# Kernel tuning notes

Measured on AMD Instinct MI355X. Metric: run time of the kernel, lower is better.

Reference implementation:

```python
import jax, jax.numpy as jnp
import numpy as np

H = 100  # hidden size
EPS = 1e-5  # BatchNorm1d default eps


def setup_inputs() -> dict:
    key = jax.random.key(0)
    ks = jax.random.split(key, 9)
    s_ih = 1.0 / np.sqrt(H)
    inp = {
        "x": jax.random.normal(ks[0], (16, 4096, 40), dtype=jnp.float32),
        "W_ih": jax.random.uniform(ks[1], (4 * H, 40), jnp.float32, -s_ih, s_ih),
        "W_hh": jax.random.uniform(ks[2], (4 * H, H), jnp.float32, -s_ih, s_ih),
        "b_ih": jax.random.uniform(ks[3], (4 * H,), jnp.float32, -s_ih, s_ih),
        "b_hh": jax.random.uniform(ks[4], (4 * H,), jnp.float32, -s_ih, s_ih),
        "W1": jax.random.uniform(ks[5], (H, H), jnp.float32, -s_ih, s_ih),
        "b1": jax.random.uniform(ks[6], (H,), jnp.float32, -s_ih, s_ih),
        "gamma": jnp.ones((H,), jnp.float32),
        "beta": jnp.zeros((H,), jnp.float32),
        "W2": jax.random.uniform(ks[7], (40, H), jnp.float32, -s_ih, s_ih),
        "b2": jax.random.uniform(ks[8], (40,), jnp.float32, -s_ih, s_ih),
    }
    return inp


def _lstm_last_h(x, W_ih, W_hh, b_ih, b_hh):
    # x: [B, T, 40] -> precompute input projections for all timesteps
    B = x.shape[0]
    xg = jnp.einsum("bti,gi->tbg", x, W_ih) + b_ih + b_hh  # [T, B, 4H]
    W_hh_T = W_hh.T  # [H, 4H]

    def step(carry, xg_t):
        h, c = carry
        z = xg_t + h @ W_hh_T  # [B, 4H]
        i = jax.nn.sigmoid(z[:, 0 * H:1 * H])
        f = jax.nn.sigmoid(z[:, 1 * H:2 * H])
        g = jnp.tanh(z[:, 2 * H:3 * H])
        o = jax.nn.sigmoid(z[:, 3 * H:4 * H])
        c = f * c + i * g
        h = o * jnp.tanh(c)
        return (h, c), None

    h0 = jnp.zeros((B, H), x.dtype)
    c0 = jnp.zeros((B, H), x.dtype)
    (h_T, _), _ = jax.lax.scan(step, (h0, c0), xg)
    return h_T  # [B, H] == out[:, -1, :]


def reference(x, W_ih, W_hh, b_ih, b_hh, W1, b1, gamma, beta, W2, b2):
    h = _lstm_last_h(x, W_ih, W_hh, b_ih, b_hh)  # [B, H]
    y = h @ W1.T + b1  # Linear(100, 100)
    # BatchNorm1d in training mode: batch statistics, biased variance
    mu = jnp.mean(y, axis=0)
    var = jnp.mean((y - mu) ** 2, axis=0)
    y = (y - mu) * jax.lax.rsqrt(var + EPS) * gamma + beta
    y = y @ W2.T + b2  # Linear(100, 40)
    return y.reshape(-1, 10, 4)
```

## Files before the change

kernel.cpp:

```cpp
#include <hip/hip_runtime.h>
#include <cstddef>
#include <cstdint>

#define H100  100
#define G4    400
#define BATCH 16
#define TTOT  4096
#define NIN   40

__device__ __forceinline__ float fast_rcp(float x) { return __builtin_amdgcn_rcpf(x); }

__device__ __forceinline__ float gate_act(float z, bool is_g) {
    float m = is_g ? -2.0f : -1.0f;
    float e = __expf(m * z);
    float r = fast_rcp(1.0f + e);
    return is_g ? (2.0f * r - 1.0f) : r;
}
__device__ __forceinline__ float tanh_fast(float x) {
    float e = __expf(-2.0f * x);
    float r = fast_rcp(1.0f + e);
    return 2.0f * r - 1.0f;
}

__global__ __launch_bounds__(256) void xg_kernel(
    const float* __restrict__ x, const float* __restrict__ W_ih,
    const float* __restrict__ b_ih, const float* __restrict__ b_hh,
    float* __restrict__ xg, int t0, int steps, int chunkT)
{
    __shared__ float W_lds[NIN * G4];
    __shared__ float x_lds[16 * NIN];
    __shared__ float bias_lds[G4];

    int tid = threadIdx.x;
    int blocks_per_b = (steps + 15) >> 4;
    int b   = blockIdx.x / blocks_per_b;
    int tt  = blockIdx.x % blocks_per_b;
    int lt0 = tt * 16;
    int ntau = min(16, steps - lt0);

    for (int p = tid; p < NIN * G4; p += 256) {
        int g = p / NIN, i = p % NIN;
        W_lds[i * G4 + g] = W_ih[p];
    }
    for (int p = tid; p < G4; p += 256) bias_lds[p] = b_ih[p] + b_hh[p];
    const float* xsrc = x + ((size_t)b * TTOT + (size_t)(t0 + lt0)) * NIN;
    for (int p = tid; p < ntau * NIN; p += 256) x_lds[p] = xsrc[p];
    __syncthreads();

    int ntask = ntau * G4;
    for (int p = tid; p < ntask; p += 256) {
        int tau = p / G4, g = p % G4;
        float acc = bias_lds[g];
        #pragma unroll
        for (int i = 0; i < NIN; i++)
            acc = fmaf(x_lds[tau * NIN + i], W_lds[i * G4 + g], acc);
        xg[((size_t)b * chunkT + (size_t)(lt0 + tau)) * G4 + g] = acc;
    }
}

using h2_t = decltype(__builtin_amdgcn_cvt_pkrtz(0.0f, 0.0f));

__device__ __forceinline__ int h2i(h2_t v) { int r; __builtin_memcpy(&r, &v, 4); return r; }
__device__ __forceinline__ h2_t i2h(int v) { h2_t r; __builtin_memcpy(&r, &v, 4); return r; }

#if __has_builtin(__builtin_amdgcn_fdot2)
__device__ __forceinline__ float fdot2(h2_t a, h2_t b, float c) {
    return __builtin_amdgcn_fdot2(a, b, c, false);
}
#else
__device__ __forceinline__ float fdot2(h2_t a, h2_t b, float c) {
    float d;
    asm("v_dot2_f32_f16 %0, %1, %2, %3" : "=v"(d) : "v"(a), "v"(b), "v"(c));
    return d;
}
#endif

#define PIN2(a, b) asm volatile("" : "+v"(a), "+v"(b))

__global__ __launch_bounds__(256)
__attribute__((amdgpu_waves_per_eu(1, 1)))
void lstm_kernel(
    const float* __restrict__ xg, const float* __restrict__ W_hh,
    float* __restrict__ hc, int t0, int steps, int chunkT)
{
    __shared__ float a_lds[2][G4];

    const int x = threadIdx.x;
    const int b = blockIdx.x;
    const int l = x & 63;
    const bool hasB = (x < G4 - 256);
    const int  rA = x;
    const int  rB = hasB ? (x + 256) : 0;

    const float2* wra2 = (const float2*)(W_hh + (size_t)rA * H100);
    const float2* wrb2 = (const float2*)(W_hh + (size_t)rB * H100);
#define LDW(q) \
    int wa##q = h2i(__builtin_amdgcn_cvt_pkrtz(wra2[q].x, wra2[q].y)); \
    int wb##q = h2i(__builtin_amdgcn_cvt_pkrtz(wrb2[q].x, wrb2[q].y)); \
    PIN2(wa##q, wb##q);
    LDW(0)  LDW(1)  LDW(2)  LDW(3)  LDW(4)  LDW(5)  LDW(6)  LDW(7)
    LDW(8)  LDW(9)  LDW(10) LDW(11) LDW(12) LDW(13) LDW(14) LDW(15)
    LDW(16) LDW(17) LDW(18) LDW(19) LDW(20) LDW(21) LDW(22) LDW(23)
    LDW(24) LDW(25) LDW(26) LDW(27) LDW(28) LDW(29) LDW(30) LDW(31)
    LDW(32) LDW(33) LDW(34) LDW(35) LDW(36) LDW(37) LDW(38) LDW(39)
    LDW(40) LDW(41) LDW(42) LDW(43) LDW(44) LDW(45) LDW(46) LDW(47)
    LDW(48) LDW(49)
#undef LDW

    float* hch = hc;
    float* hcc = hc + BATCH * H100;

    float h0 = 0.f, h1 = 0.f, c0 = 0.f, c1 = 0.f;
    int hpi = 0;
    if (l < 50) {
        if (t0 != 0) {
            float2 hv = ((const float2*)(hch + b * H100))[l];
            float2 cv = ((const float2*)(hcc + b * H100))[l];
            h0 = hv.x; h1 = hv.y; c0 = cv.x; c1 = cv.y;
        }
        hpi = h2i(__builtin_amdgcn_cvt_pkrtz(h0, h1));
    }

    const float* xgb = xg + (size_t)b * chunkT * G4;
    float xcA = xgb[rA];
    float xcB = hasB ? xgb[rB] : 0.0f;

    const bool is_gA = (x >= 200) && (x < 300);
    const bool is_gB = (x < 44);

#define RLH2(src, idx) i2h(__builtin_amdgcn_readlane((src), (idx)))
#define DOTQ(q, aA, aB) { const h2_t u = RLH2(hpi, q); \
    aA = fdot2(i2h(wa##q), u, aA); \
    aB = fdot2(i2h(wb##q), u, aB); }

    #pragma unroll 1
    for (int t = 0; t < steps; t++) {
        float nxA = 0.f, nxB = 0.f;
        if (t + 1 < steps) {
            const float* p = xgb + (size_t)(t + 1) * G4;
            nxA = p[rA];
            nxB = p[rB];
        }

        float aA0 = 0, aA1 = 0, aB0 = 0, aB1 = 0;
        DOTQ(0,  aA0, aB0) DOTQ(1,  aA1, aB1) DOTQ(2,  aA0, aB0) DOTQ(3,  aA1, aB1)
        DOTQ(4,  aA0, aB0) DOTQ(5,  aA1, aB1) DOTQ(6,  aA0, aB0) DOTQ(7,  aA1, aB1)
        DOTQ(8,  aA0, aB0) DOTQ(9,  aA1, aB1) DOTQ(10, aA0, aB0) DOTQ(11, aA1, aB1)
        DOTQ(12, aA0, aB0) DOTQ(13, aA1, aB1) DOTQ(14, aA0, aB0) DOTQ(15, aA1, aB1)
        DOTQ(16, aA0, aB0) DOTQ(17, aA1, aB1) DOTQ(18, aA0, aB0) DOTQ(19, aA1, aB1)
        DOTQ(20, aA0, aB0) DOTQ(21, aA1, aB1) DOTQ(22, aA0, aB0) DOTQ(23, aA1, aB1)
        DOTQ(24, aA0, aB0) DOTQ(25, aA1, aB1) DOTQ(26, aA0, aB0) DOTQ(27, aA1, aB1)
        DOTQ(28, aA0, aB0) DOTQ(29, aA1, aB1) DOTQ(30, aA0, aB0) DOTQ(31, aA1, aB1)
        DOTQ(32, aA0, aB0) DOTQ(33, aA1, aB1) DOTQ(34, aA0, aB0) DOTQ(35, aA1, aB1)
        DOTQ(36, aA0, aB0) DOTQ(37, aA1, aB1) DOTQ(38, aA0, aB0) DOTQ(39, aA1, aB1)
        DOTQ(40, aA0, aB0) DOTQ(41, aA1, aB1) DOTQ(42, aA0, aB0) DOTQ(43, aA1, aB1)
        DOTQ(44, aA0, aB0) DOTQ(45, aA1, aB1) DOTQ(46, aA0, aB0) DOTQ(47, aA1, aB1)
        DOTQ(48, aA0, aB0) DOTQ(49, aA1, aB1)

        float zA = xcA + (aA0 + aA1);
        float zB = xcB + (aB0 + aB1);

        const int par = t & 1;
        a_lds[par][rA] = gate_act(zA, is_gA);
        if (hasB) a_lds[par][x + 256] = gate_act(zB, is_gB);
        __syncthreads();

        if (l < 50) {
            const float* ab = a_lds[par];
            float2 gi = ((const float2*)(ab))[l];
            float2 gf = ((const float2*)(ab + 100))[l];
            float2 gg = ((const float2*)(ab + 200))[l];
            float2 go = ((const float2*)(ab + 300))[l];
            c0 = fmaf(gf.x, c0, gi.x * gg.x);
            c1 = fmaf(gf.y, c1, gi.y * gg.y);
            h0 = go.x * tanh_fast(c0);
            h1 = go.y * tanh_fast(c1);
            hpi = h2i(__builtin_amdgcn_cvt_pkrtz(h0, h1));
        }
        xcA = nxA; xcB = nxB;
    }

    if (x < 64 && l < 50) {
        float2 hv = make_float2(h0, h1);
        float2 cv = make_float2(c0, c1);
        ((float2*)(hch + b * H100))[l] = hv;
        ((float2*)(hcc + b * H100))[l] = cv;
    }
#undef DOTQ
#undef RLH2
}

__global__ __launch_bounds__(256) void head_kernel(
    const float* __restrict__ hc, const float* __restrict__ W1,
    const float* __restrict__ b1, const float* __restrict__ gamma,
    const float* __restrict__ beta, const float* __restrict__ W2,
    const float* __restrict__ b2, float* __restrict__ out)
{
    __shared__ float h_s[BATCH * H100];
    __shared__ float W1_s[H100 * 101];
    __shared__ float y1_s[BATCH * H100];
    __shared__ float W2_s[40 * 101];
    __shared__ float scale_s[H100], shift_s[H100];

    int tid = threadIdx.x;
    for (int p = tid; p < BATCH * H100; p += 256) h_s[p] = hc[p];
    for (int p = tid; p < H100 * H100; p += 256)
        W1_s[(p / H100) * 101 + p % H100] = W1[p];
    for (int p = tid; p < 40 * H100; p += 256)
        W2_s[(p / H100) * 101 + p % H100] = W2[p];
    __syncthreads();

    for (int p = tid; p < BATCH * H100; p += 256) {
        int b = p / H100, j = p % H100;
        float acc = b1[j];
        for (int k = 0; k < H100; k++)
            acc = fmaf(h_s[b * H100 + k], W1_s[j * 101 + k], acc);
        y1_s[b * H100 + j] = acc;
    }
    __syncthreads();

    if (tid < H100) {
        float mu = 0.0f;
        for (int b = 0; b < BATCH; b++) mu += y1_s[b * H100 + tid];
        mu *= (1.0f / BATCH);
        float var = 0.0f;
        for (int b = 0; b < BATCH; b++) {
            float d = y1_s[b * H100 + tid] - mu;
            var = fmaf(d, d, var);
        }
        var *= (1.0f / BATCH);
        float sc = gamma[tid] * rsqrtf(var + 1e-5f);
        scale_s[tid] = sc;
        shift_s[tid] = beta[tid] - mu * sc;
    }
    __syncthreads();

    for (int p = tid; p < BATCH * 40; p += 256) {
        int b = p / 40, o = p % 40;
        float acc = b2[o];
        for (int k = 0; k < H100; k++)
            acc = fmaf(fmaf(y1_s[b * H100 + k], scale_s[k], shift_s[k]),
                       W2_s[o * 101 + k], acc);
        out[p] = acc;
    }
}

extern "C" void kernel_launch(void* const* d_in, const int* in_sizes, int n_in,
                              void* d_out, int out_size, void* d_ws, size_t ws_size,
                              hipStream_t stream)
{
    const float* x     = (const float*)d_in[0];
    const float* W_ih  = (const float*)d_in[1];
    const float* W_hh  = (const float*)d_in[2];
    const float* b_ih  = (const float*)d_in[3];
    const float* b_hh  = (const float*)d_in[4];
    const float* W1    = (const float*)d_in[5];
    const float* b1    = (const float*)d_in[6];
    const float* gamma = (const float*)d_in[7];
    const float* beta  = (const float*)d_in[8];
    const float* W2    = (const float*)d_in[9];
    const float* b2    = (const float*)d_in[10];
    float* out = (float*)d_out;

    float* hc = (float*)d_ws;
    float* xg = (float*)((char*)d_ws + 16384);
    size_t avail    = ws_size > 16384 ? ws_size - 16384 : 0;
    size_t per_step = (size_t)BATCH * G4 * sizeof(float);
    size_t ct       = (avail / per_step) & ~(size_t)15;
    int chunkT = ct > TTOT ? TTOT : (int)ct;
    if (chunkT < 16) chunkT = 16;

    for (int t0 = 0; t0 < TTOT; t0 += chunkT) {
        int steps = (TTOT - t0 < chunkT) ? (TTOT - t0) : chunkT;
        int bpb = (steps + 15) / 16;
        xg_kernel<<<dim3(BATCH * bpb), 256, 0, stream>>>(
            x, W_ih, b_ih, b_hh, xg, t0, steps, chunkT);
        lstm_kernel<<<dim3(BATCH), 256, 0, stream>>>(
            xg, W_hh, hc, t0, steps, chunkT);
    }
    head_kernel<<<1, 256, 0, stream>>>(hc, W1, b1, gamma, beta, W2, b2, out);
}
```

Before: 2.725 ms.

## Spread LSTM gate rows over 512 threads, one row per thread

The recurrent kernel now launches 512 threads per batch element, and each thread owns a single gate row instead of some threads owning two. This halves the dot-product chain per thread in the serial per-timestep critical path. The readlane broadcasts are software-pipelined ahead of their fdot2 uses. The cost is eight waves per block with a full barrier each step, and a 448-thread worker cutoff that leaves the last wave idle but still synchronising.

```diff
diff --git a/kernel.cpp b/kernel.cpp
--- a/kernel.cpp
+++ b/kernel.cpp
@@ -75,10 +75,9 @@
 }
 #endif
 
-#define PIN2(a, b) asm volatile("" : "+v"(a), "+v"(b))
-
-__global__ __launch_bounds__(256)
-__attribute__((amdgpu_waves_per_eu(1, 1)))
+#define PIN1(a) asm volatile("" : "+v"(a))
+
+__global__ __launch_bounds__(512, 2)
 void lstm_kernel(
     const float* __restrict__ xg, const float* __restrict__ W_hh,
     float* __restrict__ hc, int t0, int steps, int chunkT)
@@ -88,16 +87,12 @@
     const int x = threadIdx.x;
     const int b = blockIdx.x;
     const int l = x & 63;
-    const bool hasB = (x < G4 - 256);
-    const int  rA = x;
-    const int  rB = hasB ? (x + 256) : 0;
-
-    const float2* wra2 = (const float2*)(W_hh + (size_t)rA * H100);
-    const float2* wrb2 = (const float2*)(W_hh + (size_t)rB * H100);
-#define LDW(q) \
-    int wa##q = h2i(__builtin_amdgcn_cvt_pkrtz(wra2[q].x, wra2[q].y)); \
-    int wb##q = h2i(__builtin_amdgcn_cvt_pkrtz(wrb2[q].x, wrb2[q].y)); \
-    PIN2(wa##q, wb##q);
+    const bool valid  = (x < G4);
+    const bool worker = (x < 448);
+    const int  r = valid ? x : 0;
+
+    const float2* wr2 = (const float2*)(W_hh + (size_t)r * H100);
+#define LDW(q) int wa##q = h2i(__builtin_amdgcn_cvt_pkrtz(wr2[q].x, wr2[q].y)); PIN1(wa##q);
     LDW(0)  LDW(1)  LDW(2)  LDW(3)  LDW(4)  LDW(5)  LDW(6)  LDW(7)
     LDW(8)  LDW(9)  LDW(10) LDW(11) LDW(12) LDW(13) LDW(14) LDW(15)
     LDW(16) LDW(17) LDW(18) LDW(19) LDW(20) LDW(21) LDW(22) LDW(23)
@@ -122,50 +117,43 @@
     }
 
     const float* xgb = xg + (size_t)b * chunkT * G4;
-    float xcA = xgb[rA];
-    float xcB = hasB ? xgb[rB] : 0.0f;
-
-    const bool is_gA = (x >= 200) && (x < 300);
-    const bool is_gB = (x < 44);
+    float xc = valid ? xgb[r] : 0.0f;
+
+    const bool is_g = (r >= 200) && (r < 300);
 
 #define RLH2(src, idx) i2h(__builtin_amdgcn_readlane((src), (idx)))
-#define DOTQ(q, aA, aB) { const h2_t u = RLH2(hpi, q); \
-    aA = fdot2(i2h(wa##q), u, aA); \
-    aB = fdot2(i2h(wb##q), u, aB); }
+#define DOTP0(q) { a0 = fdot2(i2h(wa##q), u0, a0); \
+                   if ((q) + 2 < 50) u0 = RLH2(hpi, (q) + 2); }
+#define DOTP1(q) { a1 = fdot2(i2h(wa##q), u1, a1); \
+                   if ((q) + 2 < 50) u1 = RLH2(hpi, (q) + 2); }
 
     #pragma unroll 1
     for (int t = 0; t < steps; t++) {
-        float nxA = 0.f, nxB = 0.f;
-        if (t + 1 < steps) {
-            const float* p = xgb + (size_t)(t + 1) * G4;
-            nxA = p[rA];
-            nxB = p[rB];
-        }
-
-        float aA0 = 0, aA1 = 0, aB0 = 0, aB1 = 0;
-        DOTQ(0,  aA0, aB0) DOTQ(1,  aA1, aB1) DOTQ(2,  aA0, aB0) DOTQ(3,  aA1, aB1)
-        DOTQ(4,  aA0, aB0) DOTQ(5,  aA1, aB1) DOTQ(6,  aA0, aB0) DOTQ(7,  aA1, aB1)
-        DOTQ(8,  aA0, aB0) DOTQ(9,  aA1, aB1) DOTQ(10, aA0, aB0) DOTQ(11, aA1, aB1)
-        DOTQ(12, aA0, aB0) DOTQ(13, aA1, aB1) DOTQ(14, aA0, aB0) DOTQ(15, aA1, aB1)
-        DOTQ(16, aA0, aB0) DOTQ(17, aA1, aB1) DOTQ(18, aA0, aB0) DOTQ(19, aA1, aB1)
-        DOTQ(20, aA0, aB0) DOTQ(21, aA1, aB1) DOTQ(22, aA0, aB0) DOTQ(23, aA1, aB1)
-        DOTQ(24, aA0, aB0) DOTQ(25, aA1, aB1) DOTQ(26, aA0, aB0) DOTQ(27, aA1, aB1)
-        DOTQ(28, aA0, aB0) DOTQ(29, aA1, aB1) DOTQ(30, aA0, aB0) DOTQ(31, aA1, aB1)
-        DOTQ(32, aA0, aB0) DOTQ(33, aA1, aB1) DOTQ(34, aA0, aB0) DOTQ(35, aA1, aB1)
-        DOTQ(36, aA0, aB0) DOTQ(37, aA1, aB1) DOTQ(38, aA0, aB0) DOTQ(39, aA1, aB1)
-        DOTQ(40, aA0, aB0) DOTQ(41, aA1, aB1) DOTQ(42, aA0, aB0) DOTQ(43, aA1, aB1)
-        DOTQ(44, aA0, aB0) DOTQ(45, aA1, aB1) DOTQ(46, aA0, aB0) DOTQ(47, aA1, aB1)
-        DOTQ(48, aA0, aB0) DOTQ(49, aA1, aB1)
-
-        float zA = xcA + (aA0 + aA1);
-        float zB = xcB + (aB0 + aB1);
-
         const int par = t & 1;
-        a_lds[par][rA] = gate_act(zA, is_gA);
-        if (hasB) a_lds[par][x + 256] = gate_act(zB, is_gB);
+        if (worker) {
+            float nx = 0.f;
+            if (valid && (t + 1 < steps)) nx = xgb[(size_t)(t + 1) * G4 + r];
+
+            float a0 = 0.f, a1 = 0.f;
+            h2_t u0 = RLH2(hpi, 0);
+            h2_t u1 = RLH2(hpi, 1);
+            DOTP0(0)  DOTP1(1)  DOTP0(2)  DOTP1(3)  DOTP0(4)  DOTP1(5)
+            DOTP0(6)  DOTP1(7)  DOTP0(8)  DOTP1(9)  DOTP0(10) DOTP1(11)
+            DOTP0(12) DOTP1(13) DOTP0(14) DOTP1(15) DOTP0(16) DOTP1(17)
+            DOTP0(18) DOTP1(19) DOTP0(20) DOTP1(21) DOTP0(22) DOTP1(23)
+            DOTP0(24) DOTP1(25) DOTP0(26) DOTP1(27) DOTP0(28) DOTP1(29)
+            DOTP0(30) DOTP1(31) DOTP0(32) DOTP1(33) DOTP0(34) DOTP1(35)
+            DOTP0(36) DOTP1(37) DOTP0(38) DOTP1(39) DOTP0(40) DOTP1(41)
+            DOTP0(42) DOTP1(43) DOTP0(44) DOTP1(45) DOTP0(46) DOTP1(47)
+            DOTP0(48) DOTP1(49)
+
+            float z = xc + (a0 + a1);
+            if (valid) a_lds[par][r] = gate_act(z, is_g);
+            xc = nx;
+        }
         __syncthreads();
 
-        if (l < 50) {
+        if (worker && l < 50) {
             const float* ab = a_lds[par];
             float2 gi = ((const float2*)(ab))[l];
             float2 gf = ((const float2*)(ab + 100))[l];
@@ -177,16 +165,14 @@
             h1 = go.y * tanh_fast(c1);
             hpi = h2i(__builtin_amdgcn_cvt_pkrtz(h0, h1));
         }
-        xcA = nxA; xcB = nxB;
     }
 
     if (x < 64 && l < 50) {
-        float2 hv = make_float2(h0, h1);
-        float2 cv = make_float2(c0, c1);
-        ((float2*)(hch + b * H100))[l] = hv;
-        ((float2*)(hcc + b * H100))[l] = cv;
-    }
-#undef DOTQ
+        ((float2*)(hch + b * H100))[l] = make_float2(h0, h1);
+        ((float2*)(hcc + b * H100))[l] = make_float2(c0, c1);
+    }
+#undef DOTP0
+#undef DOTP1
 #undef RLH2
 }
 
@@ -275,7 +261,7 @@
         int bpb = (steps + 15) / 16;
         xg_kernel<<<dim3(BATCH * bpb), 256, 0, stream>>>(
             x, W_ih, b_ih, b_hh, xg, t0, steps, chunkT);
-        lstm_kernel<<<dim3(BATCH), 256, 0, stream>>>(
+        lstm_kernel<<<dim3(BATCH), 512, 0, stream>>>(
             xg, W_hh, hc, t0, steps, chunkT);
     }
     head_kernel<<<1, 256, 0, stream>>>(hc, W1, b1, gamma, beta, W2, b2, out);
```

Result: slower. 2.953 ms (+8.3%).
